# Kernel optimization log

Hardware: AMD Instinct MI355X
Metric: run time of the kernel (lower is better)

Reference implementation:

```python
import jax, jax.numpy as jnp
import numpy as np

B, S, DIM, HD = 4, 1024, 2048, 128
H = DIM // HD  # 16 heads
GN_EPS = 1e-3  # Keras GroupNormalization default epsilon


def setup_inputs() -> dict:
    key = jax.random.key(0)
    ks = jax.random.split(key, 8)
    x = jax.random.normal(ks[0], (B, S, DIM), dtype=jnp.float32)
    k = jax.random.normal(ks[1], (B, S, DIM), dtype=jnp.float32)
    v = jax.random.normal(ks[2], (B, S, DIM), dtype=jnp.float32)
    # One shared QKV projection weight per head (dict.fromkeys bug in source
    # makes Q, K, V use the SAME Dense layer). Keras Dense: y = x @ W, W:(in,out)
    Wh = jax.random.normal(ks[3], (H, HD, HD), dtype=jnp.float32) / np.sqrt(HD)
    wg_w = jax.random.normal(ks[4], (DIM, DIM), dtype=jnp.float32) / np.sqrt(DIM)
    wo_w = jax.random.normal(ks[5], (DIM, DIM), dtype=jnp.float32) / np.sqrt(DIM)
    gn_gamma = jnp.ones((DIM,), dtype=jnp.float32)
    gn_beta = jnp.zeros((DIM,), dtype=jnp.float32)
    return {"x": x, "k": k, "v": v, "Wh": Wh, "wg_w": wg_w, "wo_w": wo_w,
            "gn_gamma": gn_gamma, "gn_beta": gn_beta}


def _decay_masks(n_heads, seq_len):
    # Source: band_part(gamma**(i-j), 0, -1) then transpose ->
    # D[h, i, j] = gamma_h ** (j - i) for j <= i, else 0.
    gam = 1.0 - 2.0 ** (-5.0 - jnp.arange(n_heads, dtype=jnp.float32))  # (H,)
    idx = jnp.arange(seq_len, dtype=jnp.float32)
    expo = idx[None, :] - idx[:, None]               # (S,S): j - i
    D = jnp.where(expo[None, :, :] <= 0,
                  gam[:, None, None] ** expo[None, :, :], 0.0)  # (H,S,S)
    # TF: D /= reduce_sum(D, 1)**0.5 broadcasts row-sums along the COLUMN axis
    return D / jnp.sqrt(D.sum(axis=-1))[:, None, :]


def reference(x, k, v, Wh, wg_w, wo_w, gn_gamma, gn_beta):
    b, s, dim = x.shape
    h, hd, _ = Wh.shape
    # split last axis into contiguous per-head chunks
    xh = x.reshape(b, s, h, hd)
    kh = k.reshape(b, s, h, hd)
    vh = v.reshape(b, s, h, hd)
    # Q, K, V share the same per-head weight (faithful to dict.fromkeys)
    Q = jnp.einsum('bshd,hde->bshe', xh, Wh)
    K = jnp.einsum('bshd,hde->bshe', kh, Wh)
    V = jnp.einsum('bshd,hde->bshe', vh, Wh)
    scores = jnp.einsum('bshe,bthe->bhst', Q, K) / jnp.sqrt(jnp.float32(hd))
    Dn = _decay_masks(h, s)                          # (H,S,S)
    masked = scores * Dn[None, :, :, :]              # (B,H,S,S)
    # source reduces over axis 0 == BATCH, then abs, then clamp at 1
    A = jnp.maximum(jnp.abs(masked.sum(axis=0)), 1.0)  # (H,S,S)
    O = jnp.einsum('hst,bthe->bshe', A, V).reshape(b, s, dim)
    # GroupNormalization(groups=1): per-token layernorm over channels
    mu = O.mean(axis=-1, keepdims=True)
    var = O.var(axis=-1, keepdims=True)
    Y = (O - mu) / jnp.sqrt(var + GN_EPS) * gn_gamma + gn_beta
    W = jax.nn.relu(x @ wg_w)                        # gated branch
    return (W * Y) @ wo_w
```

## Files before the change

kernel.cpp:

```cpp
#include <hip/hip_runtime.h>
#include <math.h>

constexpr int Bc = 4, Sc = 1024, Dc = 2048, HDc = 128, Hc = 16;
constexpr int BSc = Bc * Sc;
constexpr int KQKc = Bc * HDc;
#define GN_EPS 1e-3f

typedef __bf16 bf16x8 __attribute__((ext_vector_type(8)));
typedef __bf16 bf16x4 __attribute__((ext_vector_type(4)));
typedef float f32x4 __attribute__((ext_vector_type(4)));

constexpr size_t OFF_Q   = 0;
constexpr size_t OFF_K   = OFF_Q + (size_t)Hc * Sc * KQKc / 2;
constexpr size_t OFF_VB  = OFF_K + (size_t)Hc * Sc * KQKc / 2;
constexpr size_t OFF_VT  = OFF_VB + (size_t)BSc * Dc / 2;
constexpr size_t OFF_A   = OFF_VT + (size_t)BSc * Dc / 2;
constexpr size_t OFF_O   = OFF_A + (size_t)Hc * Sc * Sc / 2;
constexpr size_t OFF_CT  = OFF_O + (size_t)BSc * Dc;
constexpr size_t OFF_PN  = OFF_CT + (size_t)Hc * Sc;
constexpr size_t OFF_XB  = OFF_PN + (size_t)Hc * Sc;
constexpr size_t OFF_WGT = OFF_XB + (size_t)BSc * Dc / 2;
constexpr size_t OFF_WOT = OFF_WGT + (size_t)Dc * Dc / 2;
constexpr size_t OFF_SUF = OFF_WOT + (size_t)Dc * Dc / 2;
constexpr size_t OFF_T   = OFF_SUF + (size_t)64 * 9 * HDc;
constexpr size_t OFF_WHT = OFF_T + (size_t)64 * 8 * HDc;
constexpr size_t OFF_KB2 = OFF_A;
constexpr size_t OFF_VB2 = OFF_A + (size_t)BSc * Dc / 2;

#define GLOAD_LDS16(gp, lp)                                               \
  __builtin_amdgcn_global_load_lds(                                       \
      (const __attribute__((address_space(1))) void*)(gp),                \
      (__attribute__((address_space(3))) void*)(lp), 16, 0, 0)


constexpr int ABUFE = 128 * 64;
constexpr int BBUFE = 128 * 64;
constexpr int MG_LDS = (3 * ABUFE + 2 * BBUFE) * 2;

template <int ASTR, int BSTR>
__device__ __forceinline__ void mfma_loop128(const __bf16* __restrict__ Abase,
                                             const __bf16* __restrict__ Bbase,
                                             const int ntk,
                                             __bf16* As, __bf16* Bs,
                                             const int wave, const int lane,
                                             f32x4 acc[4][4]) {
  const int wr = wave >> 1, wc = wave & 1;
  const int lr = lane >> 2;
  const int lkx = ((lane & 3) ^ ((lane >> 3) & 3)) * 8;
  const int rl = lane & 15, kq = lane >> 4;
  const int swo = rl * 32 + ((kq ^ ((rl >> 1) & 3)) * 8);

#define SA_(i, kt, bsel) do {                                               \
    const int ci_ = (i) * 4 + wave;                                         \
    GLOAD_LDS16(Abase + (size_t)((ci_ >> 1) * 16 + lr) * ASTR               \
                    + (kt) * 64 + (ci_ & 1) * 32 + lkx,                     \
                As + (bsel) * ABUFE + ci_ * 512);                           \
  } while (0)
#define SB_(j, kt, bsel) do {                                               \
    const int ci_ = (j) * 4 + wave;                                         \
    GLOAD_LDS16(Bbase + (size_t)((ci_ >> 1) * 16 + lr) * BSTR               \
                    + (kt) * 64 + (ci_ & 1) * 32 + lkx,                     \
                Bs + (bsel) * BBUFE + ci_ * 512);                           \
  } while (0)

  SA_(0, 0, 0); SA_(1, 0, 0); SA_(2, 0, 0); SA_(3, 0, 0);
  SB_(0, 0, 0); SB_(1, 0, 0); SB_(2, 0, 0); SB_(3, 0, 0);
  SA_(0, 1, 1); SA_(1, 1, 1); SA_(2, 1, 1); SA_(3, 1, 1);
  __builtin_amdgcn_sched_barrier(0);
  asm volatile("s_waitcnt vmcnt(4)" ::: "memory");
  __builtin_amdgcn_sched_barrier(0);
  __builtin_amdgcn_s_barrier();

  int cbA = 0;
  for (int t = 0; t < ntk; ++t) {
    const int sbA = (cbA + 2 >= 3) ? cbA - 1 : cbA + 2;
    const __bf16* Ac = As + cbA * ABUFE;
    const __bf16* Bc = Bs + (t & 1) * BBUFE;
    bf16x8 a[4][2], b[4][2];
    #pragma unroll
    for (int m = 0; m < 2; ++m)
      #pragma unroll
      for (int kc = 0; kc < 2; ++kc)
        a[m][kc] = *(const bf16x8*)&Ac[((wr * 4 + m) * 2 + kc) * 512 + swo];
    #pragma unroll
    for (int n = 0; n < 2; ++n)
      #pragma unroll
      for (int kc = 0; kc < 2; ++kc)
        b[n][kc] = *(const bf16x8*)&Bc[((wc * 4 + n) * 2 + kc) * 512 + swo];
    #pragma unroll
    for (int m = 2; m < 4; ++m)
      #pragma unroll
      for (int kc = 0; kc < 2; ++kc)
        a[m][kc] = *(const bf16x8*)&Ac[((wr * 4 + m) * 2 + kc) * 512 + swo];
    #pragma unroll
    for (int n = 2; n < 4; ++n)
      #pragma unroll
      for (int kc = 0; kc < 2; ++kc)
        b[n][kc] = *(const bf16x8*)&Bc[((wc * 4 + n) * 2 + kc) * 512 + swo];
    if (t + 1 < ntk) {
      SB_(0, t + 1, (t + 1) & 1); SB_(1, t + 1, (t + 1) & 1);
      SB_(2, t + 1, (t + 1) & 1); SB_(3, t + 1, (t + 1) & 1);
    }
    if (t + 2 < ntk) {
      SA_(0, t + 2, sbA); SA_(1, t + 2, sbA);
      SA_(2, t + 2, sbA); SA_(3, t + 2, sbA);
    }
    __builtin_amdgcn_sched_barrier(0);
    __builtin_amdgcn_s_setprio(1);
    #pragma unroll
    for (int kc = 0; kc < 2; ++kc)
      #pragma unroll
      for (int m = 0; m < 2; ++m)
        #pragma unroll
        for (int n = 0; n < 2; ++n)
          acc[m][n] = __builtin_amdgcn_mfma_f32_16x16x32_bf16(
              a[m][kc], b[n][kc], acc[m][n], 0, 0, 0);
    __builtin_amdgcn_s_setprio(0);
    __builtin_amdgcn_sched_barrier(0);
    __builtin_amdgcn_s_setprio(1);
    #pragma unroll
    for (int kc = 0; kc < 2; ++kc)
      #pragma unroll
      for (int m = 2; m < 4; ++m)
        #pragma unroll
        for (int n = 0; n < 2; ++n)
          acc[m][n] = __builtin_amdgcn_mfma_f32_16x16x32_bf16(
              a[m][kc], b[n][kc], acc[m][n], 0, 0, 0);
    __builtin_amdgcn_s_setprio(0);
    __builtin_amdgcn_sched_barrier(0);
    __builtin_amdgcn_s_setprio(1);
    #pragma unroll
    for (int kc = 0; kc < 2; ++kc)
      #pragma unroll
      for (int m = 0; m < 2; ++m)
        #pragma unroll
        for (int n = 2; n < 4; ++n)
          acc[m][n] = __builtin_amdgcn_mfma_f32_16x16x32_bf16(
              a[m][kc], b[n][kc], acc[m][n], 0, 0, 0);
    __builtin_amdgcn_s_setprio(0);
    __builtin_amdgcn_sched_barrier(0);
    __builtin_amdgcn_s_setprio(1);
    #pragma unroll
    for (int kc = 0; kc < 2; ++kc)
      #pragma unroll
      for (int m = 2; m < 4; ++m)
        #pragma unroll
        for (int n = 2; n < 4; ++n)
          acc[m][n] = __builtin_amdgcn_mfma_f32_16x16x32_bf16(
              a[m][kc], b[n][kc], acc[m][n], 0, 0, 0);
    __builtin_amdgcn_s_setprio(0);
    __builtin_amdgcn_sched_barrier(0);
    asm volatile("s_waitcnt lgkmcnt(0)" ::: "memory");
    __builtin_amdgcn_sched_barrier(0);
    if (t + 2 < ntk)
      asm volatile("s_waitcnt vmcnt(4)" ::: "memory");
    else if (t + 1 < ntk)
      asm volatile("s_waitcnt vmcnt(0)" ::: "memory");
    __builtin_amdgcn_sched_barrier(0);
    __builtin_amdgcn_s_barrier();
    cbA = (cbA + 1 >= 3) ? 0 : cbA + 1;
  }
#undef SA_
#undef SB_
}

__global__ __launch_bounds__(256) void k_tables(float* __restrict__ ct,
                                                float* __restrict__ pn) {
  int idx = blockIdx.x * 256 + threadIdx.x;
  int h = idx >> 10, t = idx & 1023;
  double gamma = 1.0 - exp2(-(double)(5 + h));
  double l2g = log2(gamma);
  double r = 1.0 / gamma;
  double rowsum = (exp2(-(double)(t + 1) * l2g) - 1.0) / (r - 1.0);
  ct[idx] = (float)(exp2((double)t * l2g) / sqrt(rowsum));
  pn[idx] = (float)exp2(-(double)t * l2g);
}

__global__ __launch_bounds__(256) void k_cast83(const float* __restrict__ s0,
                                                const float* __restrict__ s1,
                                                const float* __restrict__ s2,
                                                __bf16* __restrict__ d0,
                                                __bf16* __restrict__ d1,
                                                __bf16* __restrict__ d2) {
  const int y = blockIdx.y;
  const float* src = (y == 0) ? s0 : (y == 1) ? s1 : s2;
  __bf16* dst = (y == 0) ? d0 : (y == 1) ? d1 : d2;
  size_t i = ((size_t)blockIdx.x * 256 + threadIdx.x) * 8;
  float4 a = *(const float4*)(src + i);
  float4 b = *(const float4*)(src + i + 4);
  bf16x8 o;
  o[0] = (__bf16)a.x; o[1] = (__bf16)a.y; o[2] = (__bf16)a.z; o[3] = (__bf16)a.w;
  o[4] = (__bf16)b.x; o[5] = (__bf16)b.y; o[6] = (__bf16)b.z; o[7] = (__bf16)b.w;
  *(bf16x8*)(dst + i) = o;
}

__global__ __launch_bounds__(256) void k_castT(const float* __restrict__ src,
                                               __bf16* __restrict__ dst) {
  __shared__ float t[32][33];
  const int bx = blockIdx.x, by = blockIdx.y;
  const int tid = threadIdx.x;
  const int lx = tid & 31, ly = tid >> 5;
  #pragma unroll
  for (int r = 0; r < 32; r += 8)
    t[ly + r][lx] = src[(size_t)(by * 32 + ly + r) * Dc + bx * 32 + lx];
  __syncthreads();
  #pragma unroll
  for (int r = 0; r < 32; r += 8)
    dst[(size_t)(bx * 32 + ly + r) * Dc + by * 32 + lx] = (__bf16)t[lx][ly + r];
}

__global__ __launch_bounds__(256) void k_whT(const float* __restrict__ Wh,
                                             __bf16* __restrict__ WhT) {
  __shared__ float t[32][33];
  const int h = blockIdx.z;
  const int d0 = blockIdx.x * 32, e0 = blockIdx.y * 32;
  const int tid = threadIdx.x;
  const int lx = tid & 31, ly = tid >> 5;
  #pragma unroll
  for (int r = 0; r < 32; r += 8)
    t[ly + r][lx] = Wh[(size_t)h * HDc * HDc + (d0 + ly + r) * HDc + e0 + lx];
  __syncthreads();
  #pragma unroll
  for (int r = 0; r < 32; r += 8)
    WhT[(size_t)h * HDc * HDc + (e0 + ly + r) * HDc + d0 + lx] =
        (__bf16)t[lx][ly + r];
}

__global__ __launch_bounds__(256, 2) void k_projm(const __bf16* __restrict__ Xb,
                                                  const __bf16* __restrict__ Kb2,
                                                  const __bf16* __restrict__ Vb2,
                                                  const __bf16* __restrict__ WhT,
                                                  __bf16* __restrict__ Qo,
                                                  __bf16* __restrict__ Ko,
                                                  __bf16* __restrict__ Vo) {
  extern __shared__ __bf16 lds[];
  __bf16* As = lds;
  __bf16* Bs = lds + 3 * ABUFE;
  const int r0 = blockIdx.x * 128;
  const int h = blockIdx.y;
  const int z = blockIdx.z;
  const __bf16* src = (z == 0) ? Xb : (z == 1) ? Kb2 : Vb2;
  const int tid = threadIdx.x;
  const int wave = tid >> 6, lane = tid & 63;
  f32x4 acc[4][4] = {{}};
  mfma_loop128<Dc, HDc>(src + (size_t)r0 * Dc + h * HDc,
                        WhT + (size_t)h * HDc * HDc, 2, As, Bs, wave, lane,
                        acc);
  const int wr = wave >> 1, wc = wave & 1;
  const int rl = lane & 15, kq = lane >> 4;
  #pragma unroll
  for (int mi = 0; mi < 4; ++mi) {
    #pragma unroll
    for (int nj = 0; nj < 4; ++nj) {
      const int col = wc * 64 + nj * 16 + rl;
      #pragma unroll
      for (int r = 0; r < 4; ++r) {
        const int row = r0 + wr * 64 + mi * 16 + kq * 4 + r;
        const __bf16 v = (__bf16)acc[mi][nj][r];
        if (z == 2) {
          Vo[(size_t)row * Dc + h * HDc + col] = v;
        } else {
          const int s = row & 1023, bb = row >> 10;
          __bf16* dst = (z == 0) ? Qo : Ko;
          dst[((size_t)(h * Sc + s) * Bc + bb) * HDc + col] = v;
        }
      }
    }
  }
}

__global__ __launch_bounds__(256) void k_vt(const __bf16* __restrict__ VB,
                                            __bf16* __restrict__ Vt) {
  __shared__ float tl[32][33];
  const int bh = blockIdx.z, bb = bh >> 4, h = bh & 15;
  const int t0 = blockIdx.x * 32, e0 = blockIdx.y * 32;
  const int tid = threadIdx.x;
  const int lx = tid & 31, ly = tid >> 5;
  #pragma unroll
  for (int r = 0; r < 32; r += 8)
    tl[ly + r][lx] =
        (float)VB[(size_t)(bb * Sc + t0 + ly + r) * Dc + h * HDc + e0 + lx];
  __syncthreads();
  #pragma unroll
  for (int r = 0; r < 32; r += 8)
    Vt[((size_t)bh * HDc + e0 + ly + r) * Sc + t0 + lx] = (__bf16)tl[lx][ly + r];
}

__global__ __launch_bounds__(256) void k_vsum(const __bf16* __restrict__ VB,
                                              float* __restrict__ T) {
  const int jj = blockIdx.x, bh = blockIdx.y;
  const int bb = bh >> 4, h = bh & 15;
  const int tid = threadIdx.x;
  const int tp = tid >> 7, e = tid & 127;
  const __bf16* base =
      VB + (size_t)(bb * Sc + jj * 128 + tp * 64) * Dc + h * HDc + e;
  float a0 = 0.f, a1 = 0.f, a2 = 0.f, a3 = 0.f;
  float a4 = 0.f, a5 = 0.f, a6 = 0.f, a7 = 0.f;
  for (int t = 0; t < 64; t += 8) {
    a0 += (float)base[(size_t)(t + 0) * Dc];
    a1 += (float)base[(size_t)(t + 1) * Dc];
    a2 += (float)base[(size_t)(t + 2) * Dc];
    a3 += (float)base[(size_t)(t + 3) * Dc];
    a4 += (float)base[(size_t)(t + 4) * Dc];
    a5 += (float)base[(size_t)(t + 5) * Dc];
    a6 += (float)base[(size_t)(t + 6) * Dc];
    a7 += (float)base[(size_t)(t + 7) * Dc];
  }
  const float s = ((a0 + a1) + (a2 + a3)) + ((a4 + a5) + (a6 + a7));
  __shared__ float red[2][128];
  red[tp][e] = s;
  __syncthreads();
  if (tp == 0)
    T[((size_t)bh * 8 + jj) * HDc + e] = red[0][e] + red[1][e];
}

__global__ __launch_bounds__(128) void k_vscan(const float* __restrict__ T,
                                               float* __restrict__ SufV) {
  const int bh = blockIdx.x;
  const int e = threadIdx.x;
  float acc = 0.f;
  SufV[((size_t)bh * 9 + 8) * HDc + e] = 0.f;
  for (int jj = 7; jj >= 1; --jj) {
    acc += T[((size_t)bh * 8 + jj) * HDc + e];
    SufV[((size_t)bh * 9 + jj) * HDc + e] = acc;
  }
}

__global__ __launch_bounds__(256, 2) void k_ssm(const __bf16* __restrict__ Q,
                                                const __bf16* __restrict__ Kb,
                                                const float* __restrict__ ct,
                                                const float* __restrict__ pn,
                                                __bf16* __restrict__ A) {
  const int bx = blockIdx.x, by = blockIdx.y;
  if (bx > by) return;
  extern __shared__ __bf16 lds[];
  __bf16* As = lds;
  __bf16* Bs = lds + 3 * ABUFE;
  const int h = blockIdx.z;
  const int t0 = bx * 128, s0 = by * 128;
  const int tid = threadIdx.x;
  __bf16* Ah = A + (size_t)h * Sc * Sc;
  const int wave = tid >> 6, lane = tid & 63;
  f32x4 acc[4][4] = {{}};
  mfma_loop128<KQKc, KQKc>(Q + (size_t)(h * Sc + s0) * KQKc,
                           Kb + (size_t)(h * Sc + t0) * KQKc, KQKc / 64, As,
                           Bs, wave, lane, acc);
  const int wr = wave >> 1, wc = wave & 1;
  const int rl = lane & 15, kq = lane >> 4;
  const float rs = 0.088388347648318447f;
  #pragma unroll
  for (int mi = 0; mi < 4; ++mi) {
    #pragma unroll
    for (int nj = 0; nj < 4; ++nj) {
      const int t = t0 + wc * 64 + nj * 16 + rl;
      const float ctv = ct[h * Sc + t] * rs;
      #pragma unroll
      for (int r = 0; r < 4; ++r) {
        const int s = s0 + wr * 64 + mi * 16 + kq * 4 + r;
        float v = 1.0f;
        if (t <= s) v = fmaxf(fabsf(ctv * pn[h * Sc + s] * acc[mi][nj][r]), 1.0f);
        Ah[(size_t)s * Sc + t] = (__bf16)v;
      }
    }
  }
}

__global__ __launch_bounds__(256, 2) void k_avm(const __bf16* __restrict__ A,
                                                const __bf16* __restrict__ Vt,
                                                const float* __restrict__ SufV,
                                                float* __restrict__ O) {
  extern __shared__ __bf16 lds[];
  __bf16* As = lds;
  __bf16* Bs = lds + 3 * ABUFE;
  const int bh = blockIdx.z, bb = bh >> 4, h = bh & 15;
  const int itile = blockIdx.x;
  const int s0 = itile * 128;
  const int tid = threadIdx.x;
  const int wave = tid >> 6, lane = tid & 63;
  f32x4 acc[4][4] = {{}};
  mfma_loop128<Sc, Sc>(A + (size_t)(h * Sc + s0) * Sc,
                       Vt + (size_t)bh * HDc * Sc, (itile + 1) * 2, As, Bs,
                       wave, lane, acc);
  const int wr = wave >> 1, wc = wave & 1;
  const int rl = lane & 15, kq = lane >> 4;
  const float* sufr = SufV + ((size_t)bh * 9 + (itile + 1)) * HDc;
  #pragma unroll
  for (int mi = 0; mi < 4; ++mi) {
    #pragma unroll
    for (int nj = 0; nj < 4; ++nj) {
      const int e = wc * 64 + nj * 16 + rl;
      const float sv = sufr[e];
      #pragma unroll
      for (int r = 0; r < 4; ++r) {
        const int s = s0 + wr * 64 + mi * 16 + kq * 4 + r;
        O[(size_t)(bb * Sc + s) * Dc + h * HDc + e] = acc[mi][nj][r] + sv;
      }
    }
  }
}

__global__ __launch_bounds__(256) void k_gnorm(float* __restrict__ O,
                                               const float* __restrict__ gw,
                                               const float* __restrict__ bw) {
  const int r = blockIdx.x;
  const int tid = threadIdx.x;
  float* row = O + (size_t)r * Dc;
  const int c = tid * 4;
  float4 v0 = *(const float4*)(row + c);
  float4 v1 = *(const float4*)(row + c + 1024);
  __shared__ float red[256];
  __shared__ float sh_mu, sh_inv;
  red[tid] = v0.x + v0.y + v0.z + v0.w + v1.x + v1.y + v1.z + v1.w;
  __syncthreads();
  for (int st = 128; st > 0; st >>= 1) {
    if (tid < st) red[tid] += red[tid + st];
    __syncthreads();
  }
  if (tid == 0) sh_mu = red[0] * (1.0f / Dc);
  __syncthreads();
  const float mu = sh_mu;
  float d[8] = {v0.x - mu, v0.y - mu, v0.z - mu, v0.w - mu,
                v1.x - mu, v1.y - mu, v1.z - mu, v1.w - mu};
  float ssq = 0.f;
  #pragma unroll
  for (int i = 0; i < 8; ++i) ssq += d[i] * d[i];
  red[tid] = ssq;
  __syncthreads();
  for (int st = 128; st > 0; st >>= 1) {
    if (tid < st) red[tid] += red[tid + st];
    __syncthreads();
  }
  if (tid == 0) sh_inv = rsqrtf(red[0] * (1.0f / Dc) + GN_EPS);
  __syncthreads();
  const float inv = sh_inv;
  float4 g0 = *(const float4*)(gw + c), g1 = *(const float4*)(gw + c + 1024);
  float4 b0 = *(const float4*)(bw + c), b1 = *(const float4*)(bw + c + 1024);
  float4 o0, o1;
  o0.x = d[0] * inv * g0.x + b0.x; o0.y = d[1] * inv * g0.y + b0.y;
  o0.z = d[2] * inv * g0.z + b0.z; o0.w = d[3] * inv * g0.w + b0.w;
  o1.x = d[4] * inv * g1.x + b1.x; o1.y = d[5] * inv * g1.y + b1.y;
  o1.z = d[6] * inv * g1.z + b1.z; o1.w = d[7] * inv * g1.w + b1.w;
  *(float4*)(row + c) = o0;
  *(float4*)(row + c + 1024) = o1;
}

__global__ __launch_bounds__(256, 2) void k_mgemm(const __bf16* __restrict__ Ab,
                                                  const __bf16* __restrict__ Bt,
                                                  const float* __restrict__ Y,
                                                  __bf16* __restrict__ Gout,
                                                  float* __restrict__ Fout,
                                                  int mode) {
  extern __shared__ __bf16 lds[];
  __bf16* As = lds;
  __bf16* Bs = lds + 3 * ABUFE;
  int wid = blockIdx.y * gridDim.x + blockIdx.x;
  wid = (wid & 7) * 64 + (wid >> 3);
  const int r0 = (wid >> 4) * 128;
  const int c0 = (wid & 15) * 128;
  const int tid = threadIdx.x;
  const int wave = tid >> 6, lane = tid & 63;
  f32x4 acc[4][4] = {{}};
  mfma_loop128<Dc, Dc>(Ab + (size_t)r0 * Dc, Bt + (size_t)c0 * Dc, Dc / 64,
                       As, Bs, wave, lane, acc);
  const int wr = wave >> 1, wc = wave & 1;
  const int rl = lane & 15, kq = lane >> 4;
  #pragma unroll
  for (int mi = 0; mi < 4; ++mi) {
    #pragma unroll
    for (int nj = 0; nj < 4; ++nj) {
      const int col = c0 + wc * 64 + nj * 16 + rl;
      #pragma unroll
      for (int r = 0; r < 4; ++r) {
        const int row = r0 + wr * 64 + mi * 16 + kq * 4 + r;
        const size_t idx = (size_t)row * Dc + col;
        float v = acc[mi][nj][r];
        if (mode == 0) {
          v = fmaxf(v, 0.f) * Y[idx];
          Gout[idx] = (__bf16)v;
        } else {
          Fout[idx] = v;
        }
      }
    }
  }
}

extern "C" void kernel_launch(void* const* d_in, const int* in_sizes, int n_in,
                              void* d_out, int out_size, void* d_ws, size_t ws_size,
                              hipStream_t stream) {
  const float* x  = (const float*)d_in[0];
  const float* k  = (const float*)d_in[1];
  const float* v  = (const float*)d_in[2];
  const float* Wh = (const float*)d_in[3];
  const float* wg = (const float*)d_in[4];
  const float* wo = (const float*)d_in[5];
  const float* gg = (const float*)d_in[6];
  const float* gb = (const float*)d_in[7];
  float* ws = (float*)d_ws;
  __bf16* Q   = (__bf16*)(ws + OFF_Q);
  __bf16* Kp  = (__bf16*)(ws + OFF_K);
  __bf16* VB  = (__bf16*)(ws + OFF_VB);
  __bf16* Vt  = (__bf16*)(ws + OFF_VT);
  __bf16* A   = (__bf16*)(ws + OFF_A);
  float*  O   = ws + OFF_O;
  float*  CT  = ws + OFF_CT;
  float*  PN  = ws + OFF_PN;
  __bf16* XB  = (__bf16*)(ws + OFF_XB);
  __bf16* WGT = (__bf16*)(ws + OFF_WGT);
  __bf16* WOT = (__bf16*)(ws + OFF_WOT);
  float*  SUF = ws + OFF_SUF;
  float*  TP  = ws + OFF_T;
  __bf16* WHT = (__bf16*)(ws + OFF_WHT);
  __bf16* KB2 = (__bf16*)(ws + OFF_KB2);
  __bf16* VB2 = (__bf16*)(ws + OFF_VB2);
  __bf16* G   = (__bf16*)(ws + OFF_Q);

  static bool attr_done = false;
  if (!attr_done) {
    (void)hipFuncSetAttribute((const void*)k_mgemm,
                              hipFuncAttributeMaxDynamicSharedMemorySize,
                              MG_LDS);
    (void)hipFuncSetAttribute((const void*)k_projm,
                              hipFuncAttributeMaxDynamicSharedMemorySize,
                              MG_LDS);
    (void)hipFuncSetAttribute((const void*)k_ssm,
                              hipFuncAttributeMaxDynamicSharedMemorySize,
                              MG_LDS);
    (void)hipFuncSetAttribute((const void*)k_avm,
                              hipFuncAttributeMaxDynamicSharedMemorySize,
                              MG_LDS);
    attr_done = true;
  }

  k_tables<<<Hc * Sc / 256, 256, 0, stream>>>(CT, PN);
  k_cast83<<<dim3((BSc * Dc) / (256 * 8), 3), 256, 0, stream>>>(
      x, k, v, XB, KB2, VB2);
  k_castT<<<dim3(Dc / 32, Dc / 32), 256, 0, stream>>>(wg, WGT);
  k_castT<<<dim3(Dc / 32, Dc / 32), 256, 0, stream>>>(wo, WOT);
  k_whT<<<dim3(4, 4, Hc), 256, 0, stream>>>(Wh, WHT);
  k_projm<<<dim3(BSc / 128, Hc, 3), 256, MG_LDS, stream>>>(XB, KB2, VB2, WHT,
                                                           Q, Kp, VB);
  k_vt<<<dim3(Sc / 32, HDc / 32, Bc * Hc), 256, 0, stream>>>(VB, Vt);
  k_vsum<<<dim3(8, Bc * Hc), 256, 0, stream>>>(VB, TP);
  k_vscan<<<Bc * Hc, 128, 0, stream>>>(TP, SUF);
  k_ssm<<<dim3(Sc / 128, Sc / 128, Hc), 256, MG_LDS, stream>>>(Q, Kp, CT, PN,
                                                               A);
  k_avm<<<dim3(Sc / 128, 1, Bc * Hc), 256, MG_LDS, stream>>>(A, Vt, SUF, O);
  k_gnorm<<<BSc, 256, 0, stream>>>(O, gg, gb);
  k_mgemm<<<dim3(16, 32), 256, MG_LDS, stream>>>(XB, WGT, O, G, nullptr, 0);
  k_mgemm<<<dim3(16, 32), 256, MG_LDS, stream>>>(G, WOT, nullptr, nullptr,
                                                 (float*)d_out, 1);
}
```

Before: 376.1 us.

## Fuse groupnorm into gated GEMM, fold vsum into transpose, compact triangular grids

```diff
diff --git a/kernel.cpp b/kernel.cpp
--- a/kernel.cpp
+++ b/kernel.cpp
@@ -24,6 +24,7 @@
 constexpr size_t OFF_SUF = OFF_WOT + (size_t)Dc * Dc / 2;
 constexpr size_t OFF_T   = OFF_SUF + (size_t)64 * 9 * HDc;
 constexpr size_t OFF_WHT = OFF_T + (size_t)64 * 8 * HDc;
+constexpr size_t OFF_STAT= OFF_WHT + (size_t)Hc * HDc * HDc / 2;
 constexpr size_t OFF_KB2 = OFF_A;
 constexpr size_t OFF_VB2 = OFF_A + (size_t)BSc * Dc / 2;
 
@@ -165,7 +166,9 @@
 }
 
 __global__ __launch_bounds__(256) void k_tables(float* __restrict__ ct,
-                                                float* __restrict__ pn) {
+                                                float* __restrict__ pn,
+                                                float* __restrict__ TP,
+                                                float* __restrict__ STAT) {
   int idx = blockIdx.x * 256 + threadIdx.x;
   int h = idx >> 10, t = idx & 1023;
   double gamma = 1.0 - exp2(-(double)(5 + h));
@@ -174,6 +177,9 @@
   double rowsum = (exp2(-(double)(t + 1) * l2g) - 1.0) / (r - 1.0);
   ct[idx] = (float)(exp2((double)t * l2g) / sqrt(rowsum));
   pn[idx] = (float)exp2(-(double)t * l2g);
+  float4 z4 = {0.f, 0.f, 0.f, 0.f};
+  *(float4*)(TP + (size_t)idx * 4) = z4;
+  if (idx < BSc * 2) STAT[idx] = 0.f;
 }
 
 __global__ __launch_bounds__(256) void k_cast83(const float* __restrict__ s0,
@@ -194,10 +200,14 @@
   *(bf16x8*)(dst + i) = o;
 }
 
-__global__ __launch_bounds__(256) void k_castT(const float* __restrict__ src,
-                                               __bf16* __restrict__ dst) {
+__global__ __launch_bounds__(256) void k_castT2(const float* __restrict__ s0,
+                                                const float* __restrict__ s1,
+                                                __bf16* __restrict__ d0,
+                                                __bf16* __restrict__ d1) {
   __shared__ float t[32][33];
   const int bx = blockIdx.x, by = blockIdx.y;
+  const float* src = blockIdx.z ? s1 : s0;
+  __bf16* dst = blockIdx.z ? d1 : d0;
   const int tid = threadIdx.x;
   const int lx = tid & 31, ly = tid >> 5;
   #pragma unroll
@@ -270,48 +280,32 @@
 }
 
 __global__ __launch_bounds__(256) void k_vt(const __bf16* __restrict__ VB,
-                                            __bf16* __restrict__ Vt) {
+                                            __bf16* __restrict__ Vt,
+                                            float* __restrict__ TP) {
   __shared__ float tl[32][33];
+  __shared__ float rs[8][32];
   const int bh = blockIdx.z, bb = bh >> 4, h = bh & 15;
   const int t0 = blockIdx.x * 32, e0 = blockIdx.y * 32;
   const int tid = threadIdx.x;
   const int lx = tid & 31, ly = tid >> 5;
-  #pragma unroll
-  for (int r = 0; r < 32; r += 8)
-    tl[ly + r][lx] =
+  float ps = 0.f;
+  #pragma unroll
+  for (int r = 0; r < 32; r += 8) {
+    const float v =
         (float)VB[(size_t)(bb * Sc + t0 + ly + r) * Dc + h * HDc + e0 + lx];
+    tl[ly + r][lx] = v;
+    ps += v;
+  }
+  rs[ly][lx] = ps;
   __syncthreads();
   #pragma unroll
   for (int r = 0; r < 32; r += 8)
     Vt[((size_t)bh * HDc + e0 + ly + r) * Sc + t0 + lx] = (__bf16)tl[lx][ly + r];
-}
-
-__global__ __launch_bounds__(256) void k_vsum(const __bf16* __restrict__ VB,
-                                              float* __restrict__ T) {
-  const int jj = blockIdx.x, bh = blockIdx.y;
-  const int bb = bh >> 4, h = bh & 15;
-  const int tid = threadIdx.x;
-  const int tp = tid >> 7, e = tid & 127;
-  const __bf16* base =
-      VB + (size_t)(bb * Sc + jj * 128 + tp * 64) * Dc + h * HDc + e;
-  float a0 = 0.f, a1 = 0.f, a2 = 0.f, a3 = 0.f;
-  float a4 = 0.f, a5 = 0.f, a6 = 0.f, a7 = 0.f;
-  for (int t = 0; t < 64; t += 8) {
-    a0 += (float)base[(size_t)(t + 0) * Dc];
-    a1 += (float)base[(size_t)(t + 1) * Dc];
-    a2 += (float)base[(size_t)(t + 2) * Dc];
-    a3 += (float)base[(size_t)(t + 3) * Dc];
-    a4 += (float)base[(size_t)(t + 4) * Dc];
-    a5 += (float)base[(size_t)(t + 5) * Dc];
-    a6 += (float)base[(size_t)(t + 6) * Dc];
-    a7 += (float)base[(size_t)(t + 7) * Dc];
-  }
-  const float s = ((a0 + a1) + (a2 + a3)) + ((a4 + a5) + (a6 + a7));
-  __shared__ float red[2][128];
-  red[tp][e] = s;
-  __syncthreads();
-  if (tp == 0)
-    T[((size_t)bh * 8 + jj) * HDc + e] = red[0][e] + red[1][e];
+  if (ly == 0) {
+    float s = ((rs[0][lx] + rs[1][lx]) + (rs[2][lx] + rs[3][lx])) +
+              ((rs[4][lx] + rs[5][lx]) + (rs[6][lx] + rs[7][lx]));
+    atomicAdd(&TP[((size_t)bh * 8 + (t0 >> 7)) * HDc + e0 + lx], s);
+  }
 }
 
 __global__ __launch_bounds__(128) void k_vscan(const float* __restrict__ T,
@@ -331,13 +325,15 @@
                                                 const float* __restrict__ ct,
                                                 const float* __restrict__ pn,
                                                 __bf16* __restrict__ A) {
-  const int bx = blockIdx.x, by = blockIdx.y;
-  if (bx > by) return;
+  const int q = blockIdx.x;
+  int trow = (int)((sqrtf(8.f * q + 1.f) - 1.f) * 0.5f);
+  if (((trow + 1) * (trow + 2)) >> 1 <= q) ++trow;
+  const int tcol = q - ((trow * (trow + 1)) >> 1);
   extern __shared__ __bf16 lds[];
   __bf16* As = lds;
   __bf16* Bs = lds + 3 * ABUFE;
-  const int h = blockIdx.z;
-  const int t0 = bx * 128, s0 = by * 128;
+  const int h = blockIdx.y;
+  const int t0 = tcol * 128, s0 = trow * 128;
   const int tid = threadIdx.x;
   __bf16* Ah = A + (size_t)h * Sc * Sc;
   const int wave = tid >> 6, lane = tid & 63;
@@ -368,85 +364,59 @@
 __global__ __launch_bounds__(256, 2) void k_avm(const __bf16* __restrict__ A,
                                                 const __bf16* __restrict__ Vt,
                                                 const float* __restrict__ SufV,
-                                                float* __restrict__ O) {
+                                                float* __restrict__ O,
+                                                float* __restrict__ STAT) {
   extern __shared__ __bf16 lds[];
   __bf16* As = lds;
   __bf16* Bs = lds + 3 * ABUFE;
   const int bh = blockIdx.z, bb = bh >> 4, h = bh & 15;
-  const int itile = blockIdx.x;
-  const int s0 = itile * 128;
   const int tid = threadIdx.x;
   const int wave = tid >> 6, lane = tid & 63;
-  f32x4 acc[4][4] = {{}};
-  mfma_loop128<Sc, Sc>(A + (size_t)(h * Sc + s0) * Sc,
-                       Vt + (size_t)bh * HDc * Sc, (itile + 1) * 2, As, Bs,
-                       wave, lane, acc);
   const int wr = wave >> 1, wc = wave & 1;
   const int rl = lane & 15, kq = lane >> 4;
-  const float* sufr = SufV + ((size_t)bh * 9 + (itile + 1)) * HDc;
-  #pragma unroll
-  for (int mi = 0; mi < 4; ++mi) {
-    #pragma unroll
-    for (int nj = 0; nj < 4; ++nj) {
-      const int e = wc * 64 + nj * 16 + rl;
-      const float sv = sufr[e];
+  for (int half = 0; half < 2; ++half) {
+    const int itile = half ? 7 - (int)blockIdx.x : (int)blockIdx.x;
+    const int s0 = itile * 128;
+    f32x4 acc[4][4] = {{}};
+    mfma_loop128<Sc, Sc>(A + (size_t)(h * Sc + s0) * Sc,
+                         Vt + (size_t)bh * HDc * Sc, (itile + 1) * 2, As, Bs,
+                         wave, lane, acc);
+    const float* sufr = SufV + ((size_t)bh * 9 + (itile + 1)) * HDc;
+    #pragma unroll
+    for (int mi = 0; mi < 4; ++mi) {
       #pragma unroll
       for (int r = 0; r < 4; ++r) {
         const int s = s0 + wr * 64 + mi * 16 + kq * 4 + r;
-        O[(size_t)(bb * Sc + s) * Dc + h * HDc + e] = acc[mi][nj][r] + sv;
+        const size_t orow = (size_t)(bb * Sc + s);
+        float vs = 0.f, vq = 0.f;
+        #pragma unroll
+        for (int nj = 0; nj < 4; ++nj) {
+          const int e = wc * 64 + nj * 16 + rl;
+          const float v = acc[mi][nj][r] + sufr[e];
+          O[orow * Dc + h * HDc + e] = v;
+          vs += v;
+          vq += v * v;
+        }
+        #pragma unroll
+        for (int m = 1; m < 16; m <<= 1) {
+          vs += __shfl_xor(vs, m);
+          vq += __shfl_xor(vq, m);
+        }
+        if (rl == 0) {
+          atomicAdd(&STAT[orow * 2], vs);
+          atomicAdd(&STAT[orow * 2 + 1], vq);
+        }
       }
     }
   }
-}
-
-__global__ __launch_bounds__(256) void k_gnorm(float* __restrict__ O,
-                                               const float* __restrict__ gw,
-                                               const float* __restrict__ bw) {
-  const int r = blockIdx.x;
-  const int tid = threadIdx.x;
-  float* row = O + (size_t)r * Dc;
-  const int c = tid * 4;
-  float4 v0 = *(const float4*)(row + c);
-  float4 v1 = *(const float4*)(row + c + 1024);
-  __shared__ float red[256];
-  __shared__ float sh_mu, sh_inv;
-  red[tid] = v0.x + v0.y + v0.z + v0.w + v1.x + v1.y + v1.z + v1.w;
-  __syncthreads();
-  for (int st = 128; st > 0; st >>= 1) {
-    if (tid < st) red[tid] += red[tid + st];
-    __syncthreads();
-  }
-  if (tid == 0) sh_mu = red[0] * (1.0f / Dc);
-  __syncthreads();
-  const float mu = sh_mu;
-  float d[8] = {v0.x - mu, v0.y - mu, v0.z - mu, v0.w - mu,
-                v1.x - mu, v1.y - mu, v1.z - mu, v1.w - mu};
-  float ssq = 0.f;
-  #pragma unroll
-  for (int i = 0; i < 8; ++i) ssq += d[i] * d[i];
-  red[tid] = ssq;
-  __syncthreads();
-  for (int st = 128; st > 0; st >>= 1) {
-    if (tid < st) red[tid] += red[tid + st];
-    __syncthreads();
-  }
-  if (tid == 0) sh_inv = rsqrtf(red[0] * (1.0f / Dc) + GN_EPS);
-  __syncthreads();
-  const float inv = sh_inv;
-  float4 g0 = *(const float4*)(gw + c), g1 = *(const float4*)(gw + c + 1024);
-  float4 b0 = *(const float4*)(bw + c), b1 = *(const float4*)(bw + c + 1024);
-  float4 o0, o1;
-  o0.x = d[0] * inv * g0.x + b0.x; o0.y = d[1] * inv * g0.y + b0.y;
-  o0.z = d[2] * inv * g0.z + b0.z; o0.w = d[3] * inv * g0.w + b0.w;
-  o1.x = d[4] * inv * g1.x + b1.x; o1.y = d[5] * inv * g1.y + b1.y;
-  o1.z = d[6] * inv * g1.z + b1.z; o1.w = d[7] * inv * g1.w + b1.w;
-  *(float4*)(row + c) = o0;
-  *(float4*)(row + c + 1024) = o1;
 }
 
 __global__ __launch_bounds__(256, 2) void k_mgemm(const __bf16* __restrict__ Ab,
                                                   const __bf16* __restrict__ Bt,
                                                   const float* __restrict__ Y,
+                                                  const float* __restrict__ gw,
+                                                  const float* __restrict__ bw,
+                                                  const float* __restrict__ STAT,
                                                   __bf16* __restrict__ Gout,
                                                   float* __restrict__ Fout,
                                                   int mode) {
@@ -464,21 +434,34 @@
                        As, Bs, wave, lane, acc);
   const int wr = wave >> 1, wc = wave & 1;
   const int rl = lane & 15, kq = lane >> 4;
-  #pragma unroll
-  for (int mi = 0; mi < 4; ++mi) {
-    #pragma unroll
-    for (int nj = 0; nj < 4; ++nj) {
-      const int col = c0 + wc * 64 + nj * 16 + rl;
+  if (mode == 0) {
+    #pragma unroll
+    for (int mi = 0; mi < 4; ++mi) {
       #pragma unroll
       for (int r = 0; r < 4; ++r) {
         const int row = r0 + wr * 64 + mi * 16 + kq * 4 + r;
-        const size_t idx = (size_t)row * Dc + col;
-        float v = acc[mi][nj][r];
-        if (mode == 0) {
-          v = fmaxf(v, 0.f) * Y[idx];
-          Gout[idx] = (__bf16)v;
-        } else {
-          Fout[idx] = v;
+        const float mu = STAT[(size_t)row * 2] * (1.0f / Dc);
+        const float va = STAT[(size_t)row * 2 + 1] * (1.0f / Dc) - mu * mu;
+        const float inv = rsqrtf(va + GN_EPS);
+        #pragma unroll
+        for (int nj = 0; nj < 4; ++nj) {
+          const int col = c0 + wc * 64 + nj * 16 + rl;
+          const size_t idx = (size_t)row * Dc + col;
+          const float yv = (Y[idx] - mu) * inv * gw[col] + bw[col];
+          Gout[idx] = (__bf16)(fmaxf(acc[mi][nj][r], 0.f) * yv);
+        }
+      }
+    }
+  } else {
+    #pragma unroll
+    for (int mi = 0; mi < 4; ++mi) {
+      #pragma unroll
+      for (int nj = 0; nj < 4; ++nj) {
+        const int col = c0 + wc * 64 + nj * 16 + rl;
+        #pragma unroll
+        for (int r = 0; r < 4; ++r) {
+          const int row = r0 + wr * 64 + mi * 16 + kq * 4 + r;
+          Fout[(size_t)row * Dc + col] = acc[mi][nj][r];
         }
       }
     }
@@ -511,6 +494,7 @@
   float*  SUF = ws + OFF_SUF;
   float*  TP  = ws + OFF_T;
   __bf16* WHT = (__bf16*)(ws + OFF_WHT);
+  float*  STAT= ws + OFF_STAT;
   __bf16* KB2 = (__bf16*)(ws + OFF_KB2);
   __bf16* VB2 = (__bf16*)(ws + OFF_VB2);
   __bf16* G   = (__bf16*)(ws + OFF_Q);
@@ -532,22 +516,20 @@
     attr_done = true;
   }
 
-  k_tables<<<Hc * Sc / 256, 256, 0, stream>>>(CT, PN);
+  k_tables<<<Hc * Sc / 256, 256, 0, stream>>>(CT, PN, TP, STAT);
   k_cast83<<<dim3((BSc * Dc) / (256 * 8), 3), 256, 0, stream>>>(
       x, k, v, XB, KB2, VB2);
-  k_castT<<<dim3(Dc / 32, Dc / 32), 256, 0, stream>>>(wg, WGT);
-  k_castT<<<dim3(Dc / 32, Dc / 32), 256, 0, stream>>>(wo, WOT);
+  k_castT2<<<dim3(Dc / 32, Dc / 32, 2), 256, 0, stream>>>(wg, wo, WGT, WOT);
   k_whT<<<dim3(4, 4, Hc), 256, 0, stream>>>(Wh, WHT);
   k_projm<<<dim3(BSc / 128, Hc, 3), 256, MG_LDS, stream>>>(XB, KB2, VB2, WHT,
                                                            Q, Kp, VB);
-  k_vt<<<dim3(Sc / 32, HDc / 32, Bc * Hc), 256, 0, stream>>>(VB, Vt);
-  k_vsum<<<dim3(8, Bc * Hc), 256, 0, stream>>>(VB, TP);
+  k_vt<<<dim3(Sc / 32, HDc / 32, Bc * Hc), 256, 0, stream>>>(VB, Vt, TP);
   k_vscan<<<Bc * Hc, 128, 0, stream>>>(TP, SUF);
-  k_ssm<<<dim3(Sc / 128, Sc / 128, Hc), 256, MG_LDS, stream>>>(Q, Kp, CT, PN,
-                                                               A);
-  k_avm<<<dim3(Sc / 128, 1, Bc * Hc), 256, MG_LDS, stream>>>(A, Vt, SUF, O);
-  k_gnorm<<<BSc, 256, 0, stream>>>(O, gg, gb);
-  k_mgemm<<<dim3(16, 32), 256, MG_LDS, stream>>>(XB, WGT, O, G, nullptr, 0);
+  k_ssm<<<dim3(36, Hc), 256, MG_LDS, stream>>>(Q, Kp, CT, PN, A);
+  k_avm<<<dim3(4, 1, Bc * Hc), 256, MG_LDS, stream>>>(A, Vt, SUF, O, STAT);
+  k_mgemm<<<dim3(16, 32), 256, MG_LDS, stream>>>(XB, WGT, O, gg, gb, STAT, G,
+                                                 nullptr, 0);
   k_mgemm<<<dim3(16, 32), 256, MG_LDS, stream>>>(G, WOT, nullptr, nullptr,
+                                                 nullptr, nullptr, nullptr,
                                                  (float*)d_out, 1);
 }
```

After: 364.9 us. 1.03x faster.
